# Optimization experiments

Hardware: AMD Instinct MI355X
Metric: run time of the kernel (lower is better)

The kernel has to match this reference:

```python
import jax, jax.numpy as jnp
import numpy as np

NUM_SEGMENTS = 196  # superpixels
C_OUT = 224 // 4    # conv_proj out channels = img_size // 4 = 56


def setup_inputs() -> dict:
    key = jax.random.key(0)
    k1, k2, k3, k4 = jax.random.split(key, 4)
    B, C, H, Wd = 32, 3, 224, 224
    X = jax.random.normal(k1, (B, C, H, Wd), dtype=jnp.float32)
    seg_map = jax.random.randint(k2, (B, H, Wd), 0, NUM_SEGMENTS, dtype=jnp.int32)
    # Conv2d(3, 56, kernel_size=1) == pointwise linear over channels
    W = jax.random.normal(k3, (C_OUT, C), dtype=jnp.float32) * 0.1
    b = jax.random.normal(k4, (C_OUT,), dtype=jnp.float32) * 0.01
    return {"X": X, "seg_map": seg_map, "W": W, "b": b}


def reference(X, seg_map, W, b):
    B, C, H, Wd = X.shape
    # 1x1 conv projection: (B,C,H,W) -> (B,C_OUT,H,W)
    x_emb = jnp.einsum('bchw,oc->bohw', X, W) + b[None, :, None, None]
    # flatten spatial dims: (B, HW, C_OUT)
    feats = x_emb.reshape(B, C_OUT, H * Wd).transpose(0, 2, 1)
    seg = seg_map.reshape(B, H * Wd)
    # per-image segment mean over pixels
    seg_sum = jax.vmap(
        lambda f, s: jax.ops.segment_sum(f, s, num_segments=NUM_SEGMENTS)
    )(feats, seg)  # (B, NUM_SEGMENTS, C_OUT)
    counts = jax.vmap(
        lambda s: jax.ops.segment_sum(jnp.ones(s.shape, jnp.float32), s,
                                      num_segments=NUM_SEGMENTS)
    )(seg)  # (B, NUM_SEGMENTS)
    return seg_sum / jnp.maximum(counts, 1.0)[..., None]
```

## Files before the change

### kernel.cpp

```cpp
#include <hip/hip_runtime.h>
#include <hip/hip_bf16.h>

#define NSEG 196
#define C_OUT 56
#define B_IMG 32
#define HW (224 * 224)


__global__ void __launch_bounds__(256) spm_accum_kernel(
    const float* __restrict__ X,
    const int* __restrict__ seg,
    float* __restrict__ ws)
{
    __shared__ float acc[NSEG * 4];
    const int tid = threadIdx.x;
    for (int i = tid; i < NSEG * 4; i += blockDim.x) acc[i] = 0.0f;
    __syncthreads();

    const int b = blockIdx.x;
    const float* Xb = X + (size_t)b * 3 * HW;
    const int* segb = seg + (size_t)b * HW;

    const float4* x0p = (const float4*)(Xb);
    const float4* x1p = (const float4*)(Xb + HW);
    const float4* x2p = (const float4*)(Xb + 2 * HW);
    const int4* sp = (const int4*)(segb);

    const int nvec = HW / 4;
    const int stride = gridDim.y * blockDim.x;
    for (int v = blockIdx.y * blockDim.x + tid; v < nvec; v += stride) {
        int4 s4 = sp[v];
        float4 x0 = x0p[v];
        float4 x1 = x1p[v];
        float4 x2 = x2p[v];

        atomicAdd(&acc[s4.x * 4 + 0], x0.x);
        atomicAdd(&acc[s4.x * 4 + 1], x1.x);
        atomicAdd(&acc[s4.x * 4 + 2], x2.x);
        atomicAdd(&acc[s4.x * 4 + 3], 1.0f);

        atomicAdd(&acc[s4.y * 4 + 0], x0.y);
        atomicAdd(&acc[s4.y * 4 + 1], x1.y);
        atomicAdd(&acc[s4.y * 4 + 2], x1.y * 0.0f + x2.y);
        atomicAdd(&acc[s4.y * 4 + 3], 1.0f);

        atomicAdd(&acc[s4.z * 4 + 0], x0.z);
        atomicAdd(&acc[s4.z * 4 + 1], x1.z);
        atomicAdd(&acc[s4.z * 4 + 2], x2.z);
        atomicAdd(&acc[s4.z * 4 + 3], 1.0f);

        atomicAdd(&acc[s4.w * 4 + 0], x0.w);
        atomicAdd(&acc[s4.w * 4 + 1], x1.w);
        atomicAdd(&acc[s4.w * 4 + 2], x2.w);
        atomicAdd(&acc[s4.w * 4 + 3], 1.0f);
    }
    __syncthreads();

    float* wsb = ws + (size_t)b * NSEG * 4;
    for (int i = tid; i < NSEG * 4; i += blockDim.x) {
        atomicAdd(&wsb[i], acc[i]);
    }
}

__global__ void __launch_bounds__(256) spm_project_kernel(
    const float* __restrict__ ws,
    const float* __restrict__ Wm,
    const float* __restrict__ bias,
    float* __restrict__ out)
{
    const int total = B_IMG * NSEG * C_OUT;
    int idx = blockIdx.x * blockDim.x + threadIdx.x;
    if (idx >= total) return;

    int o = idx % C_OUT;
    int bs = idx / C_OUT;

    const float* a = ws + (size_t)bs * 4;
    float s0 = a[0], s1 = a[1], s2 = a[2], cnt = a[3];
    float inv = 1.0f / fmaxf(cnt, 1.0f);

    float r = (Wm[o * 3 + 0] * s0 + Wm[o * 3 + 1] * s1 + Wm[o * 3 + 2] * s2) * inv
              + bias[o];
    out[idx] = r;
}

extern "C" void kernel_launch(void* const* d_in, const int* in_sizes, int n_in,
                              void* d_out, int out_size, void* d_ws, size_t ws_size,
                              hipStream_t stream) {
    const float* X = (const float*)d_in[0];
    const int* seg = (const int*)d_in[1];
    const float* Wm = (const float*)d_in[2];
    const float* bias = (const float*)d_in[3];
    float* out = (float*)d_out;
    float* ws = (float*)d_ws;

    const size_t ws_bytes = (size_t)B_IMG * NSEG * 4 * sizeof(float);
    hipMemsetAsync(ws, 0, ws_bytes, stream);

    dim3 grid1(B_IMG, 16);
    spm_accum_kernel<<<grid1, 256, 0, stream>>>(X, seg, ws);

    const int total = B_IMG * NSEG * C_OUT;
    int blocks2 = (total + 255) / 256;
    spm_project_kernel<<<blocks2, 256, 0, stream>>>(ws, Wm, bias, out);
}
```

Baseline: 49.81 us.

## Replace global atomics and memset with per-chunk partials and fused finalize reduction

Each accumulation block now writes its shared-memory histogram to its own partial slot instead of doing global atomicAdds, so the memset launch is no longer needed. A new per-image finalize kernel sums the 16 chunk partials in shared memory and applies the projection, with weights and bias staged in LDS. Each block also processes a contiguous chunk rather than a grid stride. This removes one launch and the global atomic contention, but the finalize runs on only 32 blocks, which may underuse the GPU.

```diff
diff --git a/kernel.cpp b/kernel.cpp
--- a/kernel.cpp
+++ b/kernel.cpp
@@ -5,19 +5,23 @@
 #define C_OUT 56
 #define B_IMG 32
 #define HW (224 * 224)
+#define NCHUNK 16
+#define NVEC (HW / 4)
+#define VPC (NVEC / NCHUNK)
 
 
 __global__ void __launch_bounds__(256) spm_accum_kernel(
     const float* __restrict__ X,
     const int* __restrict__ seg,
-    float* __restrict__ ws)
+    float* __restrict__ partial)
 {
     __shared__ float acc[NSEG * 4];
     const int tid = threadIdx.x;
-    for (int i = tid; i < NSEG * 4; i += blockDim.x) acc[i] = 0.0f;
+    for (int i = tid; i < NSEG * 4; i += 256) acc[i] = 0.0f;
     __syncthreads();
 
     const int b = blockIdx.x;
+    const int chunk = blockIdx.y;
     const float* Xb = X + (size_t)b * 3 * HW;
     const int* segb = seg + (size_t)b * HW;
 
@@ -26,9 +30,8 @@
     const float4* x2p = (const float4*)(Xb + 2 * HW);
     const int4* sp = (const int4*)(segb);
 
-    const int nvec = HW / 4;
-    const int stride = gridDim.y * blockDim.x;
-    for (int v = blockIdx.y * blockDim.x + tid; v < nvec; v += stride) {
+    const int vend = (chunk + 1) * VPC;
+    for (int v = chunk * VPC + tid; v < vend; v += 256) {
         int4 s4 = sp[v];
         float4 x0 = x0p[v];
         float4 x1 = x1p[v];
@@ -41,7 +44,7 @@
 
         atomicAdd(&acc[s4.y * 4 + 0], x0.y);
         atomicAdd(&acc[s4.y * 4 + 1], x1.y);
-        atomicAdd(&acc[s4.y * 4 + 2], x1.y * 0.0f + x2.y);
+        atomicAdd(&acc[s4.y * 4 + 2], x2.y);
         atomicAdd(&acc[s4.y * 4 + 3], 1.0f);
 
         atomicAdd(&acc[s4.z * 4 + 0], x0.z);
@@ -56,32 +59,47 @@
     }
     __syncthreads();
 
-    float* wsb = ws + (size_t)b * NSEG * 4;
-    for (int i = tid; i < NSEG * 4; i += blockDim.x) {
-        atomicAdd(&wsb[i], acc[i]);
-    }
+    float* dst = partial + ((size_t)b * NCHUNK + chunk) * (NSEG * 4);
+    for (int i = tid; i < NSEG * 4; i += 256) dst[i] = acc[i];
 }
 
-__global__ void __launch_bounds__(256) spm_project_kernel(
-    const float* __restrict__ ws,
+__global__ void __launch_bounds__(256) spm_finalize_kernel(
+    const float* __restrict__ partial,
     const float* __restrict__ Wm,
     const float* __restrict__ bias,
     float* __restrict__ out)
 {
-    const int total = B_IMG * NSEG * C_OUT;
-    int idx = blockIdx.x * blockDim.x + threadIdx.x;
-    if (idx >= total) return;
+    __shared__ float acc[NSEG * 4];
+    __shared__ float Ws[C_OUT * 3];
+    __shared__ float bs[C_OUT];
 
-    int o = idx % C_OUT;
-    int bs = idx / C_OUT;
+    const int tid = threadIdx.x;
+    const int b = blockIdx.x;
 
-    const float* a = ws + (size_t)bs * 4;
-    float s0 = a[0], s1 = a[1], s2 = a[2], cnt = a[3];
-    float inv = 1.0f / fmaxf(cnt, 1.0f);
+    if (tid < C_OUT * 3) Ws[tid] = Wm[tid];
+    if (tid < C_OUT) bs[tid] = bias[tid];
 
-    float r = (Wm[o * 3 + 0] * s0 + Wm[o * 3 + 1] * s1 + Wm[o * 3 + 2] * s2) * inv
-              + bias[o];
-    out[idx] = r;
+    const float* src = partial + (size_t)b * NCHUNK * (NSEG * 4);
+    for (int i = tid; i < NSEG * 4; i += 256) {
+        float s = 0.0f;
+        #pragma unroll
+        for (int c = 0; c < NCHUNK; ++c) s += src[c * (NSEG * 4) + i];
+        acc[i] = s;
+    }
+    __syncthreads();
+
+    float* outb = out + (size_t)b * NSEG * C_OUT;
+    for (int idx = tid; idx < NSEG * C_OUT; idx += 256) {
+        int sg = idx / C_OUT;
+        int o = idx - sg * C_OUT;
+        float s0 = acc[sg * 4 + 0];
+        float s1 = acc[sg * 4 + 1];
+        float s2 = acc[sg * 4 + 2];
+        float cnt = acc[sg * 4 + 3];
+        float inv = 1.0f / fmaxf(cnt, 1.0f);
+        outb[idx] = (Ws[o * 3 + 0] * s0 + Ws[o * 3 + 1] * s1 + Ws[o * 3 + 2] * s2) * inv
+                    + bs[o];
+    }
 }
 
 extern "C" void kernel_launch(void* const* d_in, const int* in_sizes, int n_in,
@@ -94,13 +112,7 @@
     float* out = (float*)d_out;
     float* ws = (float*)d_ws;
 
-    const size_t ws_bytes = (size_t)B_IMG * NSEG * 4 * sizeof(float);
-    hipMemsetAsync(ws, 0, ws_bytes, stream);
-
-    dim3 grid1(B_IMG, 16);
+    dim3 grid1(B_IMG, NCHUNK);
     spm_accum_kernel<<<grid1, 256, 0, stream>>>(X, seg, ws);
-
-    const int total = B_IMG * NSEG * C_OUT;
-    int blocks2 = (total + 255) / 256;
-    spm_project_kernel<<<blocks2, 256, 0, stream>>>(ws, Wm, bias, out);
+    spm_finalize_kernel<<<B_IMG, 256, 0, stream>>>(ws, Wm, bias, out);
 }
```

Measured after the change: 47.26 us. 5.1% less time.
